# Performance work log

Measured on AMD Instinct MI355X. Metric: run time of the kernel, lower is better.

Reference implementation:

```python
import jax, jax.numpy as jnp
import numpy as np

B, N, D, E, C = 8, 4096, 1024, 512, 4096


def setup_inputs() -> dict:
    key = jax.random.key(0)
    k1, k2, k3 = jax.random.split(key, 3)
    x = jax.random.normal(k1, (B, N, D), dtype=jnp.float32)
    # xavier_normal_ scale for an (input_dim, codebook_dim) matrix
    scale = (2.0 / (D + E)) ** 0.5
    random_projection = jax.random.normal(k2, (D, E), dtype=jnp.float32) * scale
    codebook = jax.random.normal(k3, (C, E), dtype=jnp.float32)
    return {"x": x, "random_projection": random_projection, "codebook": codebook}


def _l2norm(v, eps=1e-12):
    # matches torch.nn.functional.normalize(p=2): v / max(||v||, eps)
    return v / jnp.maximum(jnp.linalg.norm(v, axis=-1, keepdims=True), eps)


def reference(x, random_projection, codebook):
    # project: b n d, d e -> b n e
    proj = jnp.einsum("bnd,de->bne", x, random_projection)
    pn = _l2norm(proj)            # [B, N, E], unit vectors
    cn = _l2norm(codebook)        # [C, E],   unit vectors
    # For unit vectors, ||p - c||^2 = 2 - 2 * <p, c>, so
    # argmin_c cdist == argmax_c cosine similarity (same indices as torch code).
    sim = jnp.einsum("bne,ce->bnc", pn, cn)  # [B, N, C]
    xq = jnp.argmax(sim, axis=-1).astype(jnp.int32)  # [B, N]
    return xq
```

## Files before the change

### kernel.cpp

```cpp
#include <hip/hip_runtime.h>
#include <math.h>


typedef _Float16 half8 __attribute__((ext_vector_type(8)));
typedef _Float16 half4 __attribute__((ext_vector_type(4)));
typedef float f32x4 __attribute__((ext_vector_type(4)));
typedef unsigned long long u64;
typedef unsigned int u32;

#define INV2048 (4.8828125e-4f)
#define MARGIN 0.03f

struct Split { _Float16 h, l; };

__device__ __forceinline__ Split split_f32(float v) {
    Split s;
    s.h = (_Float16)v;
    s.l = (_Float16)((v - (float)s.h) * 2048.0f);
    return s;
}

__device__ __forceinline__ void gl_lds16(const void* g, void* l) {
    __builtin_amdgcn_global_load_lds(
        (const __attribute__((address_space(1))) unsigned int*)g,
        (__attribute__((address_space(3))) unsigned int*)l, 16, 0, 0);
}

__device__ __forceinline__ u32 fkey(float v) {
    u32 b = __float_as_uint(v);
    return b ^ ((u32)((int)b >> 31) | 0x80000000u);
}
__device__ __forceinline__ float fkeyinv(u32 u) {
    u32 m2 = (u32)((int)u >> 31);
    return __uint_as_float(u ^ ((~m2) | 0x80000000u));
}

__global__ __launch_bounds__(256) void k_prep(const float* __restrict__ rp,
                                              _Float16* __restrict__ th,
                                              _Float16* __restrict__ tl,
                                              const float* __restrict__ cb,
                                              _Float16* __restrict__ ch,
                                              _Float16* __restrict__ cl,
                                              int* __restrict__ cnt) {
    const int t = threadIdx.x;
    if (blockIdx.x == 0 && t == 0) *cnt = 0;
    if (blockIdx.x < 128) {
        __shared__ float tile[64][65];
        const int k0 = (blockIdx.x & 15) * 64, n0 = (blockIdx.x >> 4) * 64;
        const int rr = t >> 6, cc = t & 63;
        #pragma unroll
        for (int i = 0; i < 16; ++i) {
            int r = i * 4 + rr;
            tile[r][cc] = rp[(size_t)(k0 + r) * 512 + n0 + cc];
        }
        __syncthreads();
        #pragma unroll
        for (int i = 0; i < 16; ++i) {
            int n = i * 4 + rr;
            Split s = split_f32(tile[cc][n]);
            size_t o = (size_t)(n0 + n) * 1024 + k0 + cc;
            th[o] = s.h;
            tl[o] = s.l;
        }
    } else {
        const int c = blockIdx.x - 128;
        const float* row = cb + (size_t)c * 512;
        float v0 = row[t];
        float v1 = row[t + 256];
        float ss = v0 * v0 + v1 * v1;
        #pragma unroll
        for (int o = 32; o > 0; o >>= 1) ss += __shfl_down(ss, o, 64);
        __shared__ float wsum[4];
        if ((t & 63) == 0) wsum[t >> 6] = ss;
        __syncthreads();
        float s = 1.0f / fmaxf(sqrtf(wsum[0] + wsum[1] + wsum[2] + wsum[3]), 1e-12f);
        Split s0 = split_f32(v0 * s);
        ch[(size_t)c * 512 + t] = s0.h;
        cl[(size_t)c * 512 + t] = s0.l;
        Split s1 = split_f32(v1 * s);
        ch[(size_t)c * 512 + t + 256] = s1.h;
        cl[(size_t)c * 512 + t + 256] = s1.l;
    }
}

__global__ __launch_bounds__(256, 2) void k_gemm1(const float* __restrict__ X,
                                                  const _Float16* __restrict__ Bh,
                                                  const _Float16* __restrict__ Bl,
                                                  _Float16* __restrict__ Ph,
                                                  _Float16* __restrict__ Pl) {
    __shared__ _Float16 sAh[128 * 64], sAl[128 * 64];
    __shared__ _Float16 sBh[128 * 64], sBl[128 * 64];
    const int t = threadIdx.x;
    const int bid = blockIdx.x;
    const int logical = (bid & 7) * 128 + (bid >> 3);
    const int nb = logical & 3;
    const int mb = logical >> 2;
    const int lane = t & 63, w = t >> 6;
    const int quad = lane >> 4, l15 = lane & 15;
    const int wm = w >> 1, wn = w & 1;

    f32x4 acc[4][4], acc2[4][4];
    const f32x4 z = {0.f, 0.f, 0.f, 0.f};
    #pragma unroll
    for (int i = 0; i < 4; ++i)
        #pragma unroll
        for (int j = 0; j < 4; ++j) { acc[i][j] = z; acc2[i][j] = z; }

    const int srow8 = lane >> 3;
    const int sseg = (lane & 7) ^ srow8;
    const _Float16* gBh = Bh + (size_t)(nb * 128 + w * 32 + srow8) * 1024 + sseg * 8;
    const _Float16* gBl = Bl + (size_t)(nb * 128 + w * 32 + srow8) * 1024 + sseg * 8;

    const int xrow = t >> 1;
    const int xk8 = (t & 1) * 4;
    const float* gX = X + (size_t)(mb * 128 + xrow) * 1024 + xk8 * 8;
    _Float16* wAh = &sAh[xrow * 64];
    _Float16* wAl = &sAl[xrow * 64];
    const int xswz = xrow & 7;

    for (int ks = 0; ks < 16; ++ks) {
        const int ko = ks * 64;
        __syncthreads();
        #pragma unroll
        for (int c = 0; c < 4; ++c) {
            gl_lds16(gBh + ko + (size_t)(c * 8) * 1024, &sBh[(w * 32 + c * 8) * 64]);
            gl_lds16(gBl + ko + (size_t)(c * 8) * 1024, &sBl[(w * 32 + c * 8) * 64]);
        }
        #pragma unroll
        for (int j = 0; j < 4; ++j) {
            float4 v0 = *(const float4*)(gX + ko + j * 8);
            float4 v1 = *(const float4*)(gX + ko + j * 8 + 4);
            Split s0 = split_f32(v0.x), s1 = split_f32(v0.y);
            Split s2 = split_f32(v0.z), s3 = split_f32(v0.w);
            Split s4 = split_f32(v1.x), s5 = split_f32(v1.y);
            Split s6 = split_f32(v1.z), s7 = split_f32(v1.w);
            half8 hv, lv;
            hv[0] = s0.h; hv[1] = s1.h; hv[2] = s2.h; hv[3] = s3.h;
            hv[4] = s4.h; hv[5] = s5.h; hv[6] = s6.h; hv[7] = s7.h;
            lv[0] = s0.l; lv[1] = s1.l; lv[2] = s2.l; lv[3] = s3.l;
            lv[4] = s4.l; lv[5] = s5.l; lv[6] = s6.l; lv[7] = s7.l;
            const int slot = ((xk8 + j) ^ xswz) * 8;
            *(half8*)&wAh[slot] = hv;
            *(half8*)&wAl[slot] = lv;
        }
        __syncthreads();
        #pragma unroll
        for (int phase = 0; phase < 2; ++phase) {
            const int slot = (((phase << 2) | quad) ^ (l15 & 7)) * 8;
            half8 ah[4], al[4], bh[4], bl[4];
            #pragma unroll
            for (int i = 0; i < 4; ++i) {
                ah[i] = *(const half8*)&sAh[(wm * 64 + i * 16 + l15) * 64 + slot];
                al[i] = *(const half8*)&sAl[(wm * 64 + i * 16 + l15) * 64 + slot];
                bh[i] = *(const half8*)&sBh[(wn * 64 + i * 16 + l15) * 64 + slot];
                bl[i] = *(const half8*)&sBl[(wn * 64 + i * 16 + l15) * 64 + slot];
            }
            #pragma unroll
            for (int mi = 0; mi < 4; ++mi)
                #pragma unroll
                for (int ni = 0; ni < 4; ++ni) {
                    acc[mi][ni]  = __builtin_amdgcn_mfma_f32_16x16x32_f16(ah[mi], bh[ni], acc[mi][ni], 0, 0, 0);
                    acc2[mi][ni] = __builtin_amdgcn_mfma_f32_16x16x32_f16(ah[mi], bl[ni], acc2[mi][ni], 0, 0, 0);
                    acc2[mi][ni] = __builtin_amdgcn_mfma_f32_16x16x32_f16(al[mi], bh[ni], acc2[mi][ni], 0, 0, 0);
                }
        }
    }
    #pragma unroll
    for (int mi = 0; mi < 4; ++mi)
        #pragma unroll
        for (int r = 0; r < 4; ++r) {
            int row = mb * 128 + wm * 64 + mi * 16 + quad * 4 + r;
            #pragma unroll
            for (int ni = 0; ni < 4; ++ni) {
                int col = nb * 128 + wn * 64 + ni * 16 + l15;
                float v = acc[mi][ni][r] + acc2[mi][ni][r] * INV2048;
                Split s = split_f32(v);
                Ph[(size_t)row * 512 + col] = s.h;
                Pl[(size_t)row * 512 + col] = s.l;
            }
        }
}

__global__ __launch_bounds__(512, 2) void k_sim_h(const _Float16* __restrict__ Ah,
                                                  const _Float16* __restrict__ Bh,
                                                  float* __restrict__ pv1,
                                                  int* __restrict__ pi1,
                                                  float* __restrict__ pv2) {
    __shared__ __align__(16) _Float16 sA[2][256 * 64];
    __shared__ __align__(16) _Float16 sB[2][256 * 64];
    u64* ept = (u64*)&sA[0][0];
    u32* epv = (u32*)&sB[0][0];
    const int t = threadIdx.x;
    const int cbk = blockIdx.x;
    const int mb = blockIdx.y;
    const int lane = t & 63, w = t >> 6;
    const int quad = lane >> 4, l15 = lane & 15;
    const int wm = w >> 2, wn = w & 3;

    f32x4 acc[8][4];
    const f32x4 z = {0.f, 0.f, 0.f, 0.f};
    #pragma unroll
    for (int i = 0; i < 8; ++i)
        #pragma unroll
        for (int j = 0; j < 4; ++j) acc[i][j] = z;

    const int srow8 = lane >> 3;
    const int sseg = (lane & 7) ^ srow8;
    const _Float16* gA = Ah + (size_t)(mb * 256 + w * 32 + srow8) * 512 + sseg * 8;
    const _Float16* gB = Bh + (size_t)(cbk * 256 + w * 32 + srow8) * 512 + sseg * 8;

    #pragma unroll
    for (int c = 0; c < 4; ++c) {
        gl_lds16(gA + (size_t)(c * 8) * 512, &sA[0][(w * 32 + c * 8) * 64]);
        gl_lds16(gB + (size_t)(c * 8) * 512, &sB[0][(w * 32 + c * 8) * 64]);
    }

    for (int kt = 0; kt < 8; ++kt) {
        const int cur = kt & 1;
        const _Float16* rA = &sA[cur][0];
        const _Float16* rB = &sB[cur][0];
        _Float16* pA = &sA[cur ^ 1][0];
        _Float16* pB = &sB[cur ^ 1][0];
        const size_t konext = (size_t)(kt + 1) * 64;

        asm volatile("s_waitcnt vmcnt(0)" ::: "memory");
        __builtin_amdgcn_s_barrier();
        asm volatile("" ::: "memory");

        half8 a[4][2], b[2][2];
        const int mh_[4] = {0, 0, 1, 1};
        const int nh_[4] = {0, 1, 1, 0};
        #pragma unroll
        for (int q = 0; q < 4; ++q) {
            const int mh = mh_[q], nh = nh_[q];
            if (q == 0 || q == 2) {
                #pragma unroll
                for (int i = 0; i < 4; ++i)
                    #pragma unroll
                    for (int kh = 0; kh < 2; ++kh)
                        a[i][kh] = *(const half8*)&rA[(wm * 128 + mh * 64 + i * 16 + l15) * 64
                                                     + ((((kh << 2) | quad) ^ (l15 & 7)) << 3)];
            }
            if (q != 2) {
                #pragma unroll
                for (int j = 0; j < 2; ++j)
                    #pragma unroll
                    for (int kh = 0; kh < 2; ++kh)
                        b[j][kh] = *(const half8*)&rB[(wn * 64 + nh * 32 + j * 16 + l15) * 64
                                                     + ((((kh << 2) | quad) ^ (l15 & 7)) << 3)];
            }
            if (kt < 7 && q < 2) {
                #pragma unroll
                for (int cc = 0; cc < 2; ++cc) {
                    const int c = q * 2 + cc;
                    gl_lds16(gA + konext + (size_t)(c * 8) * 512, &pA[(w * 32 + c * 8) * 64]);
                    gl_lds16(gB + konext + (size_t)(c * 8) * 512, &pB[(w * 32 + c * 8) * 64]);
                }
            }
            asm volatile("" ::: "memory");
            __builtin_amdgcn_s_barrier();
            asm volatile("s_waitcnt lgkmcnt(0)" ::: "memory");
            __builtin_amdgcn_sched_barrier(0);
            __builtin_amdgcn_s_setprio(1);
            #pragma unroll
            for (int i = 0; i < 4; ++i)
                #pragma unroll
                for (int j = 0; j < 2; ++j)
                    #pragma unroll
                    for (int kh = 0; kh < 2; ++kh)
                        acc[mh * 4 + i][nh * 2 + j] =
                            __builtin_amdgcn_mfma_f32_16x16x32_f16(a[i][kh], b[j][kh],
                                                                   acc[mh * 4 + i][nh * 2 + j], 0, 0, 0);
            __builtin_amdgcn_s_setprio(0);
            if (q < 3) {
                asm volatile("" ::: "memory");
                __builtin_amdgcn_s_barrier();
            }
        }
    }

    __syncthreads();
    #pragma unroll
    for (int mi = 0; mi < 8; ++mi)
        #pragma unroll
        for (int r = 0; r < 4; ++r) {
            u64 p1 = 0, p2 = 0;
            #pragma unroll
            for (int ni = 0; ni < 4; ++ni) {
                float v = acc[mi][ni][r];
                u32 col = cbk * 256 + wn * 64 + ni * 16 + l15;
                u64 p = ((u64)fkey(v) << 32) | (u32)(~col);
                if (p > p1) { p2 = p1; p1 = p; }
                else if (p > p2) p2 = p;
            }
            #pragma unroll
            for (int m = 1; m < 16; m <<= 1) {
                u64 q1 = __shfl_xor(p1, m, 64);
                u64 q2 = __shfl_xor(p2, m, 64);
                u64 lo = p1 < q1 ? p1 : q1;
                p1 = p1 < q1 ? q1 : p1;
                p2 = p2 < q2 ? q2 : p2;
                p2 = p2 < lo ? lo : p2;
            }
            if (l15 == 0) {
                int rloc = wm * 128 + mi * 16 + quad * 4 + r;
                ept[rloc * 4 + wn] = p1;
                epv[rloc * 4 + wn] = (u32)(p2 >> 32);
            }
        }
    __syncthreads();
    if (t < 256) {
        u64 b1 = 0, b2 = 0;
        u32 vk2 = 0;
        #pragma unroll
        for (int j = 0; j < 4; ++j) {
            u64 p = ept[t * 4 + j];
            if (p > b1) { b2 = b1; b1 = p; }
            else if (p > b2) b2 = p;
            u32 vk = epv[t * 4 + j];
            vk2 = vk > vk2 ? vk : vk2;
        }
        u32 k2 = (u32)(b2 >> 32);
        if (vk2 > k2) k2 = vk2;
        size_t o = (size_t)(mb * 256 + t) * 16 + cbk;
        pv1[o] = fkeyinv((u32)(b1 >> 32));
        pi1[o] = (int)(~(u32)b1);
        pv2[o] = fkeyinv(k2);
    }
}

__global__ __launch_bounds__(256) void k_flag(const float* __restrict__ pv1,
                                              const int* __restrict__ pi1,
                                              const float* __restrict__ pv2,
                                              int* __restrict__ out,
                                              int* __restrict__ list,
                                              int* __restrict__ cnt) {
    int r = blockIdx.x * 256 + threadIdx.x;
    if (r >= 32768) return;
    size_t base = (size_t)r * 16;
    float v1 = pv1[base], v2 = pv2[base];
    int i1 = pi1[base];
    #pragma unroll
    for (int j = 1; j < 16; ++j) {
        float ov1 = pv1[base + j], ov2 = pv2[base + j];
        int oi1 = pi1[base + j];
        if (ov1 > v1 || (ov1 == v1 && oi1 < i1)) { v2 = fmaxf(v1, ov2); v1 = ov1; i1 = oi1; }
        else v2 = fmaxf(v2, ov1);
    }
    out[r] = i1;
    if (v1 - v2 < MARGIN) {
        int p = atomicAdd(cnt, 1);
        list[p] = r;
    }
}

__global__ __launch_bounds__(256, 2) void k_sim_fix(const _Float16* __restrict__ Ah,
                                                    const _Float16* __restrict__ Al,
                                                    const _Float16* __restrict__ Bh,
                                                    const _Float16* __restrict__ Bl,
                                                    const int* __restrict__ list,
                                                    const int* __restrict__ cnt,
                                                    float* __restrict__ rpv,
                                                    int* __restrict__ rpi) {
    __shared__ _Float16 sAh[128 * 32], sAl[128 * 32], sBh[128 * 32], sBl[128 * 32];
    __shared__ int rowidx[128];
    __shared__ float pvs[128][2];
    __shared__ int   pis[128][2];
    const int count = *cnt;
    const int t = threadIdx.x;
    const int cbk = blockIdx.x;
    const int lane = t & 63, w = t >> 6;
    const int quad = lane >> 4, l15 = lane & 15;
    const int wm = w >> 1, wn = w & 1;

    const int srow = w * 32 + (lane >> 2);
    const int kcol = (lane & 3) * 8;
    const _Float16* gBh = Bh + (size_t)(cbk * 128 + srow) * 512 + kcol;
    const _Float16* gBl = Bl + (size_t)(cbk * 128 + srow) * 512 + kcol;

    for (int g = blockIdx.y; g * 128 < count; g += gridDim.y) {
        __syncthreads();
        if (t < 128) {
            int p = g * 128 + t;
            rowidx[t] = (p < count) ? list[p] : list[0];
        }
        __syncthreads();

        f32x4 acc[4][4], acc2[4][4];
        const f32x4 z = {0.f, 0.f, 0.f, 0.f};
        #pragma unroll
        for (int i = 0; i < 4; ++i)
            #pragma unroll
            for (int j = 0; j < 4; ++j) { acc[i][j] = z; acc2[i][j] = z; }

        for (int ks = 0; ks < 16; ++ks) {
            const int ko = ks * 32;
            __syncthreads();
            gl_lds16(gBh + ko, &sBh[w * 1024]);
            gl_lds16(gBh + ko + (size_t)16 * 512, &sBh[w * 1024 + 512]);
            gl_lds16(gBl + ko, &sBl[w * 1024]);
            gl_lds16(gBl + ko + (size_t)16 * 512, &sBl[w * 1024 + 512]);
            #pragma unroll
            for (int i = 0; i < 2; ++i) {
                int idx = i * 256 + t;
                int row = idx >> 2, seg = (idx & 3) * 8;
                size_t src = (size_t)rowidx[row] * 512 + ko + seg;
                *(half8*)&sAh[row * 32 + seg] = *(const half8*)(Ah + src);
                *(half8*)&sAl[row * 32 + seg] = *(const half8*)(Al + src);
            }
            __syncthreads();
            half8 ah[4], al[4], bh[4], bl[4];
            #pragma unroll
            for (int i = 0; i < 4; ++i) {
                ah[i] = *(const half8*)&sAh[(wm * 64 + i * 16 + l15) * 32 + quad * 8];
                al[i] = *(const half8*)&sAl[(wm * 64 + i * 16 + l15) * 32 + quad * 8];
                bh[i] = *(const half8*)&sBh[(wn * 64 + i * 16 + l15) * 32 + quad * 8];
                bl[i] = *(const half8*)&sBl[(wn * 64 + i * 16 + l15) * 32 + quad * 8];
            }
            #pragma unroll
            for (int mi = 0; mi < 4; ++mi)
                #pragma unroll
                for (int ni = 0; ni < 4; ++ni) {
                    acc[mi][ni]  = __builtin_amdgcn_mfma_f32_16x16x32_f16(ah[mi], bh[ni], acc[mi][ni], 0, 0, 0);
                    acc2[mi][ni] = __builtin_amdgcn_mfma_f32_16x16x32_f16(ah[mi], bl[ni], acc2[mi][ni], 0, 0, 0);
                    acc2[mi][ni] = __builtin_amdgcn_mfma_f32_16x16x32_f16(al[mi], bh[ni], acc2[mi][ni], 0, 0, 0);
                }
        }

        #pragma unroll
        for (int mi = 0; mi < 4; ++mi)
            #pragma unroll
            for (int r = 0; r < 4; ++r) {
                float bv = -INFINITY;
                int bi = 0x7fffffff;
                #pragma unroll
                for (int ni = 0; ni < 4; ++ni) {
                    float v = acc[mi][ni][r] + acc2[mi][ni][r] * INV2048;
                    int col = cbk * 128 + wn * 64 + ni * 16 + l15;
                    if (v > bv || (v == bv && col < bi)) { bv = v; bi = col; }
                }
                #pragma unroll
                for (int o = 1; o < 16; o <<= 1) {
                    float ov = __shfl_xor(bv, o, 64);
                    int oi = __shfl_xor(bi, o, 64);
                    if (ov > bv || (ov == bv && oi < bi)) { bv = ov; bi = oi; }
                }
                if (l15 == 0) {
                    int row = wm * 64 + mi * 16 + quad * 4 + r;
                    pvs[row][wn] = bv; pis[row][wn] = bi;
                }
            }
        __syncthreads();
        if (t < 128 && g * 128 + t < count) {
            float v0 = pvs[t][0], v1 = pvs[t][1];
            int i0 = pis[t][0], i1 = pis[t][1];
            bool sw = (v1 > v0) || (v1 == v0 && i1 < i0);
            size_t o = (size_t)(g * 128 + t) * 32 + cbk;
            rpv[o] = sw ? v1 : v0;
            rpi[o] = sw ? i1 : i0;
        }
    }
}

__global__ __launch_bounds__(256) void k_fix(const float* __restrict__ rpv,
                                             const int* __restrict__ rpi,
                                             const int* __restrict__ list,
                                             const int* __restrict__ cnt,
                                             int* __restrict__ out) {
    int p = blockIdx.x * 256 + threadIdx.x;
    if (p >= *cnt) return;
    size_t base = (size_t)p * 32;
    float bv = -INFINITY;
    int bi = 0x7fffffff;
    #pragma unroll
    for (int j = 0; j < 32; ++j) {
        float v = rpv[base + j];
        int ci = rpi[base + j];
        if (v > bv || (v == bv && ci < bi)) { bv = v; bi = ci; }
    }
    out[list[p]] = bi;
}

extern "C" void kernel_launch(void* const* d_in, const int* in_sizes, int n_in,
                              void* d_out, int out_size, void* d_ws, size_t ws_size,
                              hipStream_t stream) {
    const float* x  = (const float*)d_in[0];
    const float* rp = (const float*)d_in[1];
    const float* cb = (const float*)d_in[2];
    int* out = (int*)d_out;

    char* ws = (char*)d_ws;
    _Float16* cn_h   = (_Float16*)(ws);
    _Float16* cn_l   = (_Float16*)(ws + ((size_t)4 << 20));
    _Float16* rpT_h  = (_Float16*)(ws + ((size_t)8 << 20));
    _Float16* rpT_l  = (_Float16*)(ws + ((size_t)9 << 20));
    _Float16* proj_h = (_Float16*)(ws + ((size_t)10 << 20));
    _Float16* proj_l = (_Float16*)(ws + ((size_t)42 << 20));
    float*    pv1    = (float*)   (ws + ((size_t)74 << 20));
    int*      pi1    = (int*)     (ws + ((size_t)78 << 20));
    float*    pv2    = (float*)   (ws + ((size_t)82 << 20));
    float*    rpv    = (float*)   (ws + ((size_t)86 << 20));
    int*      rpi    = (int*)     (ws + ((size_t)90 << 20));
    int*      list   = (int*)     (ws + ((size_t)94 << 20));
    int*      cnt    = (int*)     (ws + ((size_t)94 << 20) + (128 << 10));

    k_prep<<<4224, 256, 0, stream>>>(rp, rpT_h, rpT_l, cb, cn_h, cn_l, cnt);
    k_gemm1<<<1024, 256, 0, stream>>>(x, rpT_h, rpT_l, proj_h, proj_l);
    k_sim_h<<<dim3(16, 128), 512, 0, stream>>>(proj_h, cn_h, pv1, pi1, pv2);
    k_flag<<<128, 256, 0, stream>>>(pv1, pi1, pv2, out, list, cnt);
    k_sim_fix<<<dim3(32, 32), 256, 0, stream>>>(proj_h, proj_l, cn_h, cn_l, list, cnt, rpv, rpi);
    k_fix<<<128, 256, 0, stream>>>(rpv, rpi, list, cnt, out);
}
```

Baseline: 610.4 us.

## Stage sim GEMM tiles in quadrant-granular chunks with two-tile lookahead

Restructures the k_sim_h main loop so that global-to-LDS loads are split into half-tile groups matched to the quadrant each MFMA phase consumes. Each group is issued as soon as its LDS region is free, reaching up to two K-tiles ahead, and partial vmcnt waits replace the full drain at the top of each tile. The intent is to hide global memory latency more fully behind the MFMA work. The cost is more complex buffer-reuse reasoning and a risk of LDS races if the barrier and waitcnt placement is wrong.

```diff
diff --git a/kernel.cpp b/kernel.cpp
--- a/kernel.cpp
+++ b/kernel.cpp
@@ -181,6 +181,47 @@
         }
 }
 
+#define BARX() do { asm volatile("" ::: "memory"); __builtin_amdgcn_s_barrier(); \
+                    asm volatile("" ::: "memory"); } while (0)
+#define LGKM0() do { asm volatile("s_waitcnt lgkmcnt(0)" ::: "memory"); \
+                     __builtin_amdgcn_sched_barrier(0); } while (0)
+
+#define READ_A(MH) do { \
+    _Pragma("unroll") \
+    for (int ii = 0; ii < 4; ++ii) { \
+        _Pragma("unroll") \
+        for (int kh = 0; kh < 2; ++kh) \
+            a[ii][kh] = *(const half8*)&rA[(wm * 128 + (MH) * 64 + ii * 16 + l15) * 64 \
+                                           + ((((kh << 2) | quad) ^ (l15 & 7)) << 3)]; \
+    } \
+} while (0)
+
+#define READ_B(BS, NH2) do { \
+    _Pragma("unroll") \
+    for (int jj = 0; jj < 2; ++jj) { \
+        _Pragma("unroll") \
+        for (int kh = 0; kh < 2; ++kh) \
+            BS[jj][kh] = *(const half8*)&rB[(wn * 64 + (NH2) * 32 + jj * 16 + l15) * 64 \
+                                            + ((((kh << 2) | quad) ^ (l15 & 7)) << 3)]; \
+    } \
+} while (0)
+
+#define MFMA_Q(MH, BS, NH2) do { \
+    __builtin_amdgcn_s_setprio(1); \
+    _Pragma("unroll") \
+    for (int ii = 0; ii < 4; ++ii) { \
+        _Pragma("unroll") \
+        for (int jj = 0; jj < 2; ++jj) { \
+            _Pragma("unroll") \
+            for (int kh = 0; kh < 2; ++kh) \
+                acc[(MH) * 4 + ii][(NH2) * 2 + jj] = \
+                    __builtin_amdgcn_mfma_f32_16x16x32_f16(a[ii][kh], BS[jj][kh], \
+                        acc[(MH) * 4 + ii][(NH2) * 2 + jj], 0, 0, 0); \
+        } \
+    } \
+    __builtin_amdgcn_s_setprio(0); \
+} while (0)
+
 __global__ __launch_bounds__(512, 2) void k_sim_h(const _Float16* __restrict__ Ah,
                                                   const _Float16* __restrict__ Bh,
                                                   float* __restrict__ pv1,
@@ -206,79 +247,64 @@
 
     const int srow8 = lane >> 3;
     const int sseg = (lane & 7) ^ srow8;
-    const _Float16* gA = Ah + (size_t)(mb * 256 + w * 32 + srow8) * 512 + sseg * 8;
-    const _Float16* gB = Bh + (size_t)(cbk * 256 + w * 32 + srow8) * 512 + sseg * 8;
-
-    #pragma unroll
-    for (int c = 0; c < 4; ++c) {
-        gl_lds16(gA + (size_t)(c * 8) * 512, &sA[0][(w * 32 + c * 8) * 64]);
-        gl_lds16(gB + (size_t)(c * 8) * 512, &sB[0][(w * 32 + c * 8) * 64]);
-    }
-
-    for (int kt = 0; kt < 8; ++kt) {
-        const int cur = kt & 1;
-        const _Float16* rA = &sA[cur][0];
-        const _Float16* rB = &sB[cur][0];
-        _Float16* pA = &sA[cur ^ 1][0];
-        _Float16* pB = &sB[cur ^ 1][0];
-        const size_t konext = (size_t)(kt + 1) * 64;
-
-        asm volatile("s_waitcnt vmcnt(0)" ::: "memory");
-        __builtin_amdgcn_s_barrier();
-        asm volatile("" ::: "memory");
-
-        half8 a[4][2], b[2][2];
-        const int mh_[4] = {0, 0, 1, 1};
-        const int nh_[4] = {0, 1, 1, 0};
-        #pragma unroll
-        for (int q = 0; q < 4; ++q) {
-            const int mh = mh_[q], nh = nh_[q];
-            if (q == 0 || q == 2) {
-                #pragma unroll
-                for (int i = 0; i < 4; ++i)
-                    #pragma unroll
-                    for (int kh = 0; kh < 2; ++kh)
-                        a[i][kh] = *(const half8*)&rA[(wm * 128 + mh * 64 + i * 16 + l15) * 64
-                                                     + ((((kh << 2) | quad) ^ (l15 & 7)) << 3)];
-            }
-            if (q != 2) {
-                #pragma unroll
-                for (int j = 0; j < 2; ++j)
-                    #pragma unroll
-                    for (int kh = 0; kh < 2; ++kh)
-                        b[j][kh] = *(const half8*)&rB[(wn * 64 + nh * 32 + j * 16 + l15) * 64
-                                                     + ((((kh << 2) | quad) ^ (l15 & 7)) << 3)];
-            }
-            if (kt < 7 && q < 2) {
-                #pragma unroll
-                for (int cc = 0; cc < 2; ++cc) {
-                    const int c = q * 2 + cc;
-                    gl_lds16(gA + konext + (size_t)(c * 8) * 512, &pA[(w * 32 + c * 8) * 64]);
-                    gl_lds16(gB + konext + (size_t)(c * 8) * 512, &pB[(w * 32 + c * 8) * 64]);
-                }
-            }
-            asm volatile("" ::: "memory");
-            __builtin_amdgcn_s_barrier();
-            asm volatile("s_waitcnt lgkmcnt(0)" ::: "memory");
+
+    auto stageA = [&](int buf, int tile, int g) {
+        #pragma unroll
+        for (int j = 0; j < 2; ++j) {
+            const int r0 = j * 128 + g * 64 + w * 8;
+            gl_lds16(Ah + (size_t)(mb * 256 + r0 + srow8) * 512 + tile * 64 + sseg * 8,
+                     &sA[buf][r0 * 64]);
+        }
+    };
+    auto stageB = [&](int buf, int tile, int g) {
+        #pragma unroll
+        for (int j = 0; j < 2; ++j) {
+            const int r0 = (w >> 2) * 64 + j * 128 + g * 32 + (w & 3) * 8;
+            gl_lds16(Bh + (size_t)(cbk * 256 + r0 + srow8) * 512 + tile * 64 + sseg * 8,
+                     &sB[buf][r0 * 64]);
+        }
+    };
+
+    stageA(0, 0, 0); stageB(0, 0, 0); stageB(0, 0, 1); stageA(0, 0, 1);
+    stageA(1, 1, 0); stageB(1, 1, 1);
+    asm volatile("s_waitcnt vmcnt(4)" ::: "memory");
+    __builtin_amdgcn_s_barrier();
+    asm volatile("" ::: "memory");
+
+    half8 a[4][2], bg[2][2], bd[2][2];
+
+    for (int i = 0; i < 4; ++i) {
+        #pragma unroll
+        for (int h = 0; h < 2; ++h) {
+            const int T = 2 * i + h;
+            const _Float16* rA = &sA[h][0];
+            const _Float16* rB = &sB[h][0];
+            const bool s01 = (T <= 6);
+            const bool s23 = (T <= 5);
+
+            READ_A(0); READ_B(bg, 0);
+            if (s01) stageA(h ^ 1, T + 1, 1);
+            BARX(); LGKM0(); MFMA_Q(0, bg, 0); BARX();
+
+            READ_B(bd, 1);
+            if (s01) stageB(h ^ 1, T + 1, 0);
+            BARX(); LGKM0(); MFMA_Q(0, bd, 1); BARX();
+
+            READ_A(1);
+            if (s23) stageA(h, T + 2, 0);
+            BARX(); LGKM0(); MFMA_Q(1, bd, 1); BARX();
+
+            if (s23) stageB(h, T + 2, 1);
+            if (s23)      { asm volatile("s_waitcnt vmcnt(4)" ::: "memory"); }
+            else if (s01) { asm volatile("s_waitcnt vmcnt(0)" ::: "memory"); }
+            BARX();
             __builtin_amdgcn_sched_barrier(0);
-            __builtin_amdgcn_s_setprio(1);
-            #pragma unroll
-            for (int i = 0; i < 4; ++i)
-                #pragma unroll
-                for (int j = 0; j < 2; ++j)
-                    #pragma unroll
-                    for (int kh = 0; kh < 2; ++kh)
-                        acc[mh * 4 + i][nh * 2 + j] =
-                            __builtin_amdgcn_mfma_f32_16x16x32_f16(a[i][kh], b[j][kh],
-                                                                   acc[mh * 4 + i][nh * 2 + j], 0, 0, 0);
-            __builtin_amdgcn_s_setprio(0);
-            if (q < 3) {
-                asm volatile("" ::: "memory");
-                __builtin_amdgcn_s_barrier();
-            }
-        }
-    }
-
+            MFMA_Q(1, bg, 0);
+            BARX();
+        }
+    }
+
+    asm volatile("s_waitcnt vmcnt(0) lgkmcnt(0)" ::: "memory");
     __syncthreads();
     #pragma unroll
     for (int mi = 0; mi < 8; ++mi)
```

Measured after the change: 610.7 us. No clear change (+0.0%).
